# Kernel optimization log

Hardware: AMD Instinct MI355X
Metric: run time of the kernel (lower is better)

## Reference

```python
import jax, jax.numpy as jnp
import numpy as np

B, T, D, H = 4096, 256, 5, 64


def setup_inputs() -> dict:
    key = jax.random.key(0)
    ks = jax.random.split(key, 11)
    s = 1.0 / np.sqrt(H)  # PyTorch default init scale
    mk = lambda k, shape: jax.random.uniform(k, shape, jnp.float32, -s, s)
    return {
        "x": jax.random.normal(ks[0], (B, T, D), jnp.float32),
        "w_ih0": mk(ks[1], (3 * H, D)),
        "w_hh0": mk(ks[2], (3 * H, H)),
        "b_ih0": mk(ks[3], (3 * H,)),
        "b_hh0": mk(ks[4], (3 * H,)),
        "w_ih1": mk(ks[5], (3 * H, H)),
        "w_hh1": mk(ks[6], (3 * H, H)),
        "b_ih1": mk(ks[7], (3 * H,)),
        "b_hh1": mk(ks[8], (3 * H,)),
        "fc_w": mk(ks[9], (1, H)),
        "fc_b": mk(ks[10], (1,)),
    }


def _gru_layer(x, w_ih, w_hh, b_ih, b_hh):
    # x: [B, T, Din] -> outputs [B, T, H]. PyTorch gate order: r, z, n.
    h_dim = w_hh.shape[1]
    xg = jnp.einsum("btd,gd->btg", x, w_ih) + b_ih  # [B, T, 3H] (one big GEMM)

    def step(h, xg_t):
        hg = h @ w_hh.T + b_hh  # [B, 3H]
        xr, xz, xn = jnp.split(xg_t, 3, axis=-1)
        hr, hz, hn = jnp.split(hg, 3, axis=-1)
        r = jax.nn.sigmoid(xr + hr)
        z = jax.nn.sigmoid(xz + hz)
        n = jnp.tanh(xn + r * hn)
        h_new = (1.0 - z) * n + z * h
        return h_new, h_new

    h0 = jnp.zeros((x.shape[0], h_dim), x.dtype)
    _, hs = jax.lax.scan(step, h0, jnp.swapaxes(xg, 0, 1))  # hs: [T, B, H]
    return jnp.swapaxes(hs, 0, 1)


def reference(x, w_ih0, w_hh0, b_ih0, b_hh0, w_ih1, w_hh1, b_ih1, b_hh1, fc_w, fc_b):
    h1 = _gru_layer(x, w_ih0, w_hh0, b_ih0, b_hh0)   # [B, T, H]
    h2 = _gru_layer(h1, w_ih1, w_hh1, b_ih1, b_hh1)  # [B, T, H]
    last = h2[:, -1, :]                               # [B, H]
    return last @ fc_w.T + fc_b                       # [B, 1]
```

## Files before the change

### kernel.cpp

```cpp
#include <hip/hip_runtime.h>
#include <hip/hip_bf16.h>


typedef __attribute__((ext_vector_type(8))) _Float16 f16x8;
typedef __attribute__((ext_vector_type(4))) float f32x4;

#define MFMA16(a, b, c) __builtin_amdgcn_mfma_f32_16x16x32_f16(a, b, c, 0, 0, 0)

#define T_SZ 256
#define HB   72
#define NLOG2E  (-1.4426950408889634f)
#define PLOG2E  ( 1.4426950408889634f)
#define N2LOG2E (-2.8853900817779268f)

__device__ __forceinline__ void load_wfrag_hi(const float* __restrict__ W, int grow,
                                              int kbase, float scale, f16x8& hi) {
#pragma unroll
    for (int j = 0; j < 8; ++j)
        hi[j] = (_Float16)(W[grow * 64 + kbase + j] * scale);
}

__global__ __launch_bounds__(1024, 1)
void gru2_16w(const float* __restrict__ x,
              const float* __restrict__ w_ih0, const float* __restrict__ w_hh0,
              const float* __restrict__ b_ih0, const float* __restrict__ b_hh0,
              const float* __restrict__ w_ih1, const float* __restrict__ w_hh1,
              const float* __restrict__ b_ih1, const float* __restrict__ b_hh1,
              const float* __restrict__ fc_w, const float* __restrict__ fc_b,
              float* __restrict__ out)
{
    __shared__ __align__(16) _Float16 xhi[T_SZ][16][8];
    __shared__ __align__(16) _Float16 h0hi[2][16][HB];
    __shared__ __align__(16) _Float16 h1hi[2][16][HB];
    __shared__ __align__(16) float    pP[2][3][64][20];
    __shared__ __align__(16) float    xnB[2][64][20];

    const int tid  = threadIdx.x;
    const int lane = tid & 63;
    const int wave = tid >> 6;
    const int grp  = wave >> 2;
    const int wl   = wave & 3;
    const int u    = lane & 15;
    const int kq   = lane >> 4;
    const int ug   = wl * 16 + u;
    const int rbase = 4 * kq;

    {
        const float* xsrc = x + (size_t)blockIdx.x * (16 * 1280);
        for (int idx = tid; idx < 16 * 1280; idx += 1024) {
            int row = idx / 1280;
            int rem = idx - row * 1280;
            int t   = rem / 5;
            int d   = rem - t * 5;
            xhi[t][row][d] = (_Float16)xsrc[idx];
        }
        for (int idx = tid; idx < T_SZ * 16; idx += 1024) {
            int t = idx >> 4, row = idx & 15;
            xhi[t][row][5] = (_Float16)0.0f;
            xhi[t][row][6] = (_Float16)0.0f;
            xhi[t][row][7] = (_Float16)0.0f;
        }
        for (int idx = tid; idx < 2 * 16 * HB; idx += 1024) {
            ((_Float16*)h0hi)[idx] = (_Float16)0.0f;
            ((_Float16*)h1hi)[idx] = (_Float16)0.0f;
        }
    }
    __syncthreads();

    if (grp == 0) {
        f16x8 wR[2], wZ[2], wN[2];
#pragma unroll
        for (int kk = 0; kk < 2; ++kk) {
            const int kb = kk * 32 + 8 * kq;
            load_wfrag_hi(w_hh0, 0 * 64 + ug, kb, NLOG2E,  wR[kk]);
            load_wfrag_hi(w_hh0, 1 * 64 + ug, kb, PLOG2E,  wZ[kk]);
            load_wfrag_hi(w_hh0, 2 * 64 + ug, kb, N2LOG2E, wN[kk]);
        }
        f16x8 bxR, bxZ;
#pragma unroll
        for (int j = 0; j < 8; ++j) { bxR[j] = (_Float16)0.0f; bxZ[j] = (_Float16)0.0f; }
        if (kq == 0) {
#pragma unroll
            for (int j = 0; j < 5; ++j) {
                bxR[j] = (_Float16)(w_ih0[(0 * 64 + ug) * 5 + j] * NLOG2E);
                bxZ[j] = (_Float16)(w_ih0[(1 * 64 + ug) * 5 + j] * PLOG2E);
            }
        }
        const float bR0  = (b_ih0[ug] + b_hh0[ug]) * NLOG2E;
        const float bZ0  = (b_ih0[64 + ug] + b_hh0[64 + ug]) * PLOG2E;
        const float bXN0 = b_ih0[128 + ug] * N2LOG2E;
        const float bHN0 = b_hh0[128 + ug] * N2LOG2E;
        float h0_own[4] = {0.f, 0.f, 0.f, 0.f};

        float xn_pro[4];
        {
            float wxn[5];
#pragma unroll
            for (int d = 0; d < 5; ++d) wxn[d] = w_ih0[(128 + ug) * 5 + d] * N2LOG2E;
#pragma unroll
            for (int r = 0; r < 4; ++r) {
                const float* xp = x + ((size_t)(blockIdx.x * 16 + rbase + r) * T_SZ) * 5;
                float vN = bXN0;
#pragma unroll
                for (int d = 0; d < 5; ++d) vN = fmaf(wxn[d], xp[d], vN);
                xn_pro[r] = vN;
            }
        }

        for (int i = 0; i <= T_SZ + 1; ++i) {
            if (i < T_SZ) {
                const int pr = (i + 1) & 1, ps = i & 1;
                f16x8 xf;
#pragma unroll
                for (int j = 0; j < 8; ++j) xf[j] = (_Float16)0.0f;
                if (kq == 0) xf = *(const f16x8*)&xhi[i][u][0];
                f16x8 ah[2];
                ah[0] = *(const f16x8*)&h0hi[pr][u][8 * kq];
                ah[1] = *(const f16x8*)&h0hi[pr][u][32 + 8 * kq];
                f32x4 aR  = {bR0, bR0, bR0, bR0};
                f32x4 aZ  = {bZ0, bZ0, bZ0, bZ0};
                f32x4 aNa = {bHN0, bHN0, bHN0, bHN0};
                f32x4 aNb = {0.f, 0.f, 0.f, 0.f};
                __builtin_amdgcn_s_setprio(1);
                aR  = MFMA16(xf, bxR, aR);
                aZ  = MFMA16(xf, bxZ, aZ);
                aNa = MFMA16(ah[0], wN[0], aNa);
                aNb = MFMA16(ah[1], wN[1], aNb);
                aR  = MFMA16(ah[0], wR[0], aR);
                aZ  = MFMA16(ah[0], wZ[0], aZ);
                aR  = MFMA16(ah[1], wR[1], aR);
                aZ  = MFMA16(ah[1], wZ[1], aZ);
                __builtin_amdgcn_s_setprio(0);
                float xn0[4];
                if (i == 0) {
#pragma unroll
                    for (int r = 0; r < 4; ++r) xn0[r] = xn_pro[r];
                } else {
                    const f32x4 q = *(const f32x4*)&xnB[i & 1][ug][rbase];
#pragma unroll
                    for (int r = 0; r < 4; ++r) xn0[r] = q[r];
                }
#pragma unroll
                for (int r = 0; r < 4; ++r) {
                    float ER = __builtin_amdgcn_exp2f(aR[r]);
                    float rg = __builtin_amdgcn_rcpf(1.0f + ER);
                    float w  = fmaf(rg, aNa[r] + aNb[r], xn0[r]);
                    float EN = __builtin_amdgcn_exp2f(w);
                    float n  = fmaf(2.0f, __builtin_amdgcn_rcpf(1.0f + EN), -1.0f);
                    float EZ = __builtin_amdgcn_exp2f(aZ[r]);
                    float hv = fmaf(EZ, h0_own[r], n) * __builtin_amdgcn_rcpf(1.0f + EZ);
                    h0_own[r] = hv;
                    h0hi[ps][rbase + r][ug] = (_Float16)hv;
                }
            }
            __syncthreads();
        }
    } else if (grp == 1) {
        f16x8 iR[2], iZ[2], iX[2];
#pragma unroll
        for (int kk = 0; kk < 2; ++kk) {
            const int kb = kk * 32 + 8 * kq;
            load_wfrag_hi(w_ih1, 0 * 64 + ug, kb, NLOG2E,  iR[kk]);
            load_wfrag_hi(w_ih1, 1 * 64 + ug, kb, PLOG2E,  iZ[kk]);
            load_wfrag_hi(w_ih1, 2 * 64 + ug, kb, N2LOG2E, iX[kk]);
        }
        const float bR1 = (b_ih1[ug] + b_hh1[ug]) * NLOG2E;
        const float bZ1 = (b_ih1[64 + ug] + b_hh1[64 + ug]) * PLOG2E;
        const float bX1 = b_ih1[128 + ug] * N2LOG2E;

        for (int i = 0; i <= T_SZ + 1; ++i) {
            if (i >= 1 && i <= T_SZ) {
                const int t = i - 1, st = t & 1;
                f16x8 ah[2];
                ah[0] = *(const f16x8*)&h0hi[st][u][8 * kq];
                ah[1] = *(const f16x8*)&h0hi[st][u][32 + 8 * kq];
                f32x4 qR = {bR1, bR1, bR1, bR1};
                f32x4 qZ = {bZ1, bZ1, bZ1, bZ1};
                f32x4 qXa = {bX1, bX1, bX1, bX1};
                f32x4 qXb = {0.f, 0.f, 0.f, 0.f};
                qR  = MFMA16(ah[0], iR[0], qR);
                qZ  = MFMA16(ah[0], iZ[0], qZ);
                qXa = MFMA16(ah[0], iX[0], qXa);
                qXb = MFMA16(ah[1], iX[1], qXb);
                qR  = MFMA16(ah[1], iR[1], qR);
                qZ  = MFMA16(ah[1], iZ[1], qZ);
#pragma unroll
                for (int r = 0; r < 4; ++r) qXa[r] += qXb[r];
                *(f32x4*)&pP[st][0][ug][rbase] = qR;
                *(f32x4*)&pP[st][1][ug][rbase] = qZ;
                *(f32x4*)&pP[st][2][ug][rbase] = qXa;
            }
            __syncthreads();
        }
    } else if (grp == 2) {
        float wxn[5];
#pragma unroll
        for (int d = 0; d < 5; ++d) wxn[d] = w_ih0[(128 + ug) * 5 + d] * N2LOG2E;
        const float bXN0 = b_ih0[128 + ug] * N2LOG2E;

        for (int i = 0; i <= T_SZ + 1; ++i) {
            if (i <= T_SZ - 2) {
                f32x4 xnv;
#pragma unroll
                for (int r = 0; r < 4; ++r) {
                    const float* xp = x + ((size_t)(blockIdx.x * 16 + rbase + r) * T_SZ + (i + 1)) * 5;
                    float vN = bXN0;
#pragma unroll
                    for (int d = 0; d < 5; ++d) vN = fmaf(wxn[d], xp[d], vN);
                    xnv[r] = vN;
                }
                *(f32x4*)&xnB[(i + 1) & 1][ug][rbase] = xnv;
            }
            __syncthreads();
        }
    } else {
        f16x8 hR[2], hZ[2], hN[2];
#pragma unroll
        for (int kk = 0; kk < 2; ++kk) {
            const int kb = kk * 32 + 8 * kq;
            load_wfrag_hi(w_hh1, 0 * 64 + ug, kb, NLOG2E,  hR[kk]);
            load_wfrag_hi(w_hh1, 1 * 64 + ug, kb, PLOG2E,  hZ[kk]);
            load_wfrag_hi(w_hh1, 2 * 64 + ug, kb, N2LOG2E, hN[kk]);
        }
        const float bN1 = b_hh1[128 + ug] * N2LOG2E;
        float h1_own[4] = {0.f, 0.f, 0.f, 0.f};

        for (int i = 0; i <= T_SZ + 1; ++i) {
            if (i >= 2) {
                const int t = i - 2, st = t & 1;
                f16x8 ah[2];
                ah[0] = *(const f16x8*)&h1hi[st ^ 1][u][8 * kq];
                ah[1] = *(const f16x8*)&h1hi[st ^ 1][u][32 + 8 * kq];
                const f32x4 qR = *(const f32x4*)&pP[st][0][ug][rbase];
                const f32x4 qZ = *(const f32x4*)&pP[st][1][ug][rbase];
                const f32x4 qX = *(const f32x4*)&pP[st][2][ug][rbase];
                f32x4 cR = {0.f, 0.f, 0.f, 0.f};
                f32x4 cZ = {0.f, 0.f, 0.f, 0.f};
                f32x4 cNa = {bN1, bN1, bN1, bN1};
                f32x4 cNb = {0.f, 0.f, 0.f, 0.f};
                __builtin_amdgcn_s_setprio(1);
                cR  = MFMA16(ah[0], hR[0], cR);
                cZ  = MFMA16(ah[0], hZ[0], cZ);
                cNa = MFMA16(ah[0], hN[0], cNa);
                cNb = MFMA16(ah[1], hN[1], cNb);
                cR  = MFMA16(ah[1], hR[1], cR);
                cZ  = MFMA16(ah[1], hZ[1], cZ);
                __builtin_amdgcn_s_setprio(0);
#pragma unroll
                for (int r = 0; r < 4; ++r) {
                    float ER = __builtin_amdgcn_exp2f(cR[r] + qR[r]);
                    float rg = __builtin_amdgcn_rcpf(1.0f + ER);
                    float w  = fmaf(rg, cNa[r] + cNb[r], qX[r]);
                    float EN = __builtin_amdgcn_exp2f(w);
                    float n  = fmaf(2.0f, __builtin_amdgcn_rcpf(1.0f + EN), -1.0f);
                    float EZ = __builtin_amdgcn_exp2f(cZ[r] + qZ[r]);
                    float hv = fmaf(EZ, h1_own[r], n) * __builtin_amdgcn_rcpf(1.0f + EZ);
                    h1_own[r] = hv;
                    h1hi[st][rbase + r][ug] = (_Float16)hv;
                }
            }
            __syncthreads();
        }
    }

    if (tid < 16) {
        float s = fc_b[0];
#pragma unroll 1
        for (int uu = 0; uu < 64; ++uu)
            s = fmaf(fc_w[uu], (float)h1hi[1][tid][uu], s);
        out[blockIdx.x * 16 + tid] = s;
    }
}

extern "C" void kernel_launch(void* const* d_in, const int* in_sizes, int n_in,
                              void* d_out, int out_size, void* d_ws, size_t ws_size,
                              hipStream_t stream) {
    const float* x     = (const float*)d_in[0];
    const float* w_ih0 = (const float*)d_in[1];
    const float* w_hh0 = (const float*)d_in[2];
    const float* b_ih0 = (const float*)d_in[3];
    const float* b_hh0 = (const float*)d_in[4];
    const float* w_ih1 = (const float*)d_in[5];
    const float* w_hh1 = (const float*)d_in[6];
    const float* b_ih1 = (const float*)d_in[7];
    const float* b_hh1 = (const float*)d_in[8];
    const float* fc_w  = (const float*)d_in[9];
    const float* fc_b  = (const float*)d_in[10];
    float* out = (float*)d_out;

    gru2_16w<<<dim3(256), dim3(1024), 0, stream>>>(x, w_ih0, w_hh0, b_ih0, b_hh0,
                                                   w_ih1, w_hh1, b_ih1, b_hh1,
                                                   fc_w, fc_b, out);
}
```

Before: 161.2 us.

## Move layer-0 input projections for all gates to the helper wave group

Layer-0 input projections for the r and z gates are now computed in fp32 by the helper group (grp 2), alongside the n gate it already handled. They are double-buffered through shared memory and loaded as the accumulator initial values, which removes two MFMAs from the serial recurrence step of layer 0. The shared-memory staging of x as fp16 and its prologue transpose are dropped, cutting startup cost. In exchange the helper group does three times the FMAs, global loads and shared-memory stores per step, and the recurrent wave reads two extra f32x4 values from LDS each step.

```diff
diff --git a/kernel.cpp b/kernel.cpp
--- a/kernel.cpp
+++ b/kernel.cpp
@@ -21,19 +21,18 @@
 }
 
 __global__ __launch_bounds__(1024, 1)
-void gru2_16w(const float* __restrict__ x,
-              const float* __restrict__ w_ih0, const float* __restrict__ w_hh0,
-              const float* __restrict__ b_ih0, const float* __restrict__ b_hh0,
-              const float* __restrict__ w_ih1, const float* __restrict__ w_hh1,
-              const float* __restrict__ b_ih1, const float* __restrict__ b_hh1,
-              const float* __restrict__ fc_w, const float* __restrict__ fc_b,
-              float* __restrict__ out)
+void gru2_slim0(const float* __restrict__ x,
+                const float* __restrict__ w_ih0, const float* __restrict__ w_hh0,
+                const float* __restrict__ b_ih0, const float* __restrict__ b_hh0,
+                const float* __restrict__ w_ih1, const float* __restrict__ w_hh1,
+                const float* __restrict__ b_ih1, const float* __restrict__ b_hh1,
+                const float* __restrict__ fc_w, const float* __restrict__ fc_b,
+                float* __restrict__ out)
 {
-    __shared__ __align__(16) _Float16 xhi[T_SZ][16][8];
     __shared__ __align__(16) _Float16 h0hi[2][16][HB];
     __shared__ __align__(16) _Float16 h1hi[2][16][HB];
     __shared__ __align__(16) float    pP[2][3][64][20];
-    __shared__ __align__(16) float    xnB[2][64][20];
+    __shared__ __align__(16) float    xA[2][3][64][20];
 
     const int tid  = threadIdx.x;
     const int lane = tid & 63;
@@ -45,25 +44,9 @@
     const int ug   = wl * 16 + u;
     const int rbase = 4 * kq;
 
-    {
-        const float* xsrc = x + (size_t)blockIdx.x * (16 * 1280);
-        for (int idx = tid; idx < 16 * 1280; idx += 1024) {
-            int row = idx / 1280;
-            int rem = idx - row * 1280;
-            int t   = rem / 5;
-            int d   = rem - t * 5;
-            xhi[t][row][d] = (_Float16)xsrc[idx];
-        }
-        for (int idx = tid; idx < T_SZ * 16; idx += 1024) {
-            int t = idx >> 4, row = idx & 15;
-            xhi[t][row][5] = (_Float16)0.0f;
-            xhi[t][row][6] = (_Float16)0.0f;
-            xhi[t][row][7] = (_Float16)0.0f;
-        }
-        for (int idx = tid; idx < 2 * 16 * HB; idx += 1024) {
-            ((_Float16*)h0hi)[idx] = (_Float16)0.0f;
-            ((_Float16*)h1hi)[idx] = (_Float16)0.0f;
-        }
+    for (int idx = tid; idx < 2 * 16 * HB; idx += 1024) {
+        ((_Float16*)h0hi)[idx] = (_Float16)0.0f;
+        ((_Float16*)h1hi)[idx] = (_Float16)0.0f;
     }
     __syncthreads();
 
@@ -76,54 +59,58 @@
             load_wfrag_hi(w_hh0, 1 * 64 + ug, kb, PLOG2E,  wZ[kk]);
             load_wfrag_hi(w_hh0, 2 * 64 + ug, kb, N2LOG2E, wN[kk]);
         }
-        f16x8 bxR, bxZ;
-#pragma unroll
-        for (int j = 0; j < 8; ++j) { bxR[j] = (_Float16)0.0f; bxZ[j] = (_Float16)0.0f; }
-        if (kq == 0) {
-#pragma unroll
-            for (int j = 0; j < 5; ++j) {
-                bxR[j] = (_Float16)(w_ih0[(0 * 64 + ug) * 5 + j] * NLOG2E);
-                bxZ[j] = (_Float16)(w_ih0[(1 * 64 + ug) * 5 + j] * PLOG2E);
-            }
-        }
-        const float bR0  = (b_ih0[ug] + b_hh0[ug]) * NLOG2E;
-        const float bZ0  = (b_ih0[64 + ug] + b_hh0[64 + ug]) * PLOG2E;
-        const float bXN0 = b_ih0[128 + ug] * N2LOG2E;
         const float bHN0 = b_hh0[128 + ug] * N2LOG2E;
         float h0_own[4] = {0.f, 0.f, 0.f, 0.f};
 
-        float xn_pro[4];
+        f32x4 proR, proZ, proX;
         {
-            float wxn[5];
-#pragma unroll
-            for (int d = 0; d < 5; ++d) wxn[d] = w_ih0[(128 + ug) * 5 + d] * N2LOG2E;
+            float wxr[5], wxz[5], wxn[5];
+#pragma unroll
+            for (int d = 0; d < 5; ++d) {
+                wxr[d] = w_ih0[(0 * 64 + ug) * 5 + d] * NLOG2E;
+                wxz[d] = w_ih0[(1 * 64 + ug) * 5 + d] * PLOG2E;
+                wxn[d] = w_ih0[(128 + ug) * 5 + d] * N2LOG2E;
+            }
+            const float bR0  = (b_ih0[ug] + b_hh0[ug]) * NLOG2E;
+            const float bZ0  = (b_ih0[64 + ug] + b_hh0[64 + ug]) * PLOG2E;
+            const float bXN0 = b_ih0[128 + ug] * N2LOG2E;
 #pragma unroll
             for (int r = 0; r < 4; ++r) {
                 const float* xp = x + ((size_t)(blockIdx.x * 16 + rbase + r) * T_SZ) * 5;
-                float vN = bXN0;
-#pragma unroll
-                for (int d = 0; d < 5; ++d) vN = fmaf(wxn[d], xp[d], vN);
-                xn_pro[r] = vN;
+                float vR = bR0, vZ = bZ0, vN = bXN0;
+#pragma unroll
+                for (int d = 0; d < 5; ++d) {
+                    float x1 = xp[d];
+                    vR = fmaf(wxr[d], x1, vR);
+                    vZ = fmaf(wxz[d], x1, vZ);
+                    vN = fmaf(wxn[d], x1, vN);
+                }
+                proR[r] = vR; proZ[r] = vZ; proX[r] = vN;
             }
         }
 
         for (int i = 0; i <= T_SZ + 1; ++i) {
             if (i < T_SZ) {
                 const int pr = (i + 1) & 1, ps = i & 1;
-                f16x8 xf;
-#pragma unroll
-                for (int j = 0; j < 8; ++j) xf[j] = (_Float16)0.0f;
-                if (kq == 0) xf = *(const f16x8*)&xhi[i][u][0];
                 f16x8 ah[2];
                 ah[0] = *(const f16x8*)&h0hi[pr][u][8 * kq];
                 ah[1] = *(const f16x8*)&h0hi[pr][u][32 + 8 * kq];
-                f32x4 aR  = {bR0, bR0, bR0, bR0};
-                f32x4 aZ  = {bZ0, bZ0, bZ0, bZ0};
-                f32x4 aNa = {bHN0, bHN0, bHN0, bHN0};
-                f32x4 aNb = {0.f, 0.f, 0.f, 0.f};
+                f32x4 aR, aZ, aNa, aNb;
+                float xn0[4];
+                if (i == 0) {
+                    aR = proR; aZ = proZ;
+#pragma unroll
+                    for (int r = 0; r < 4; ++r) xn0[r] = proX[r];
+                } else {
+                    aR = *(const f32x4*)&xA[i & 1][0][ug][rbase];
+                    aZ = *(const f32x4*)&xA[i & 1][1][ug][rbase];
+                    const f32x4 q = *(const f32x4*)&xA[i & 1][2][ug][rbase];
+#pragma unroll
+                    for (int r = 0; r < 4; ++r) xn0[r] = q[r];
+                }
+#pragma unroll
+                for (int r = 0; r < 4; ++r) { aNa[r] = bHN0; aNb[r] = 0.f; }
                 __builtin_amdgcn_s_setprio(1);
-                aR  = MFMA16(xf, bxR, aR);
-                aZ  = MFMA16(xf, bxZ, aZ);
                 aNa = MFMA16(ah[0], wN[0], aNa);
                 aNb = MFMA16(ah[1], wN[1], aNb);
                 aR  = MFMA16(ah[0], wR[0], aR);
@@ -131,15 +118,6 @@
                 aR  = MFMA16(ah[1], wR[1], aR);
                 aZ  = MFMA16(ah[1], wZ[1], aZ);
                 __builtin_amdgcn_s_setprio(0);
-                float xn0[4];
-                if (i == 0) {
-#pragma unroll
-                    for (int r = 0; r < 4; ++r) xn0[r] = xn_pro[r];
-                } else {
-                    const f32x4 q = *(const f32x4*)&xnB[i & 1][ug][rbase];
-#pragma unroll
-                    for (int r = 0; r < 4; ++r) xn0[r] = q[r];
-                }
 #pragma unroll
                 for (int r = 0; r < 4; ++r) {
                     float ER = __builtin_amdgcn_exp2f(aR[r]);
@@ -193,23 +171,37 @@
             __syncthreads();
         }
     } else if (grp == 2) {
-        float wxn[5];
-#pragma unroll
-        for (int d = 0; d < 5; ++d) wxn[d] = w_ih0[(128 + ug) * 5 + d] * N2LOG2E;
+        float wxr[5], wxz[5], wxn[5];
+#pragma unroll
+        for (int d = 0; d < 5; ++d) {
+            wxr[d] = w_ih0[(0 * 64 + ug) * 5 + d] * NLOG2E;
+            wxz[d] = w_ih0[(1 * 64 + ug) * 5 + d] * PLOG2E;
+            wxn[d] = w_ih0[(128 + ug) * 5 + d] * N2LOG2E;
+        }
+        const float bR0  = (b_ih0[ug] + b_hh0[ug]) * NLOG2E;
+        const float bZ0  = (b_ih0[64 + ug] + b_hh0[64 + ug]) * PLOG2E;
         const float bXN0 = b_ih0[128 + ug] * N2LOG2E;
 
         for (int i = 0; i <= T_SZ + 1; ++i) {
             if (i <= T_SZ - 2) {
-                f32x4 xnv;
+                f32x4 xvR, xvZ, xvN;
 #pragma unroll
                 for (int r = 0; r < 4; ++r) {
                     const float* xp = x + ((size_t)(blockIdx.x * 16 + rbase + r) * T_SZ + (i + 1)) * 5;
-                    float vN = bXN0;
-#pragma unroll
-                    for (int d = 0; d < 5; ++d) vN = fmaf(wxn[d], xp[d], vN);
-                    xnv[r] = vN;
-                }
-                *(f32x4*)&xnB[(i + 1) & 1][ug][rbase] = xnv;
+                    float vR = bR0, vZ = bZ0, vN = bXN0;
+#pragma unroll
+                    for (int d = 0; d < 5; ++d) {
+                        float x1 = xp[d];
+                        vR = fmaf(wxr[d], x1, vR);
+                        vZ = fmaf(wxz[d], x1, vZ);
+                        vN = fmaf(wxn[d], x1, vN);
+                    }
+                    xvR[r] = vR; xvZ[r] = vZ; xvN[r] = vN;
+                }
+                const int sl = (i + 1) & 1;
+                *(f32x4*)&xA[sl][0][ug][rbase] = xvR;
+                *(f32x4*)&xA[sl][1][ug][rbase] = xvZ;
+                *(f32x4*)&xA[sl][2][ug][rbase] = xvN;
             }
             __syncthreads();
         }
@@ -288,7 +280,7 @@
     const float* fc_b  = (const float*)d_in[10];
     float* out = (float*)d_out;
 
-    gru2_16w<<<dim3(256), dim3(1024), 0, stream>>>(x, w_ih0, w_hh0, b_ih0, b_hh0,
-                                                   w_ih1, w_hh1, b_ih1, b_hh1,
-                                                   fc_w, fc_b, out);
+    gru2_slim0<<<dim3(256), dim3(1024), 0, stream>>>(x, w_ih0, w_hh0, b_ih0, b_hh0,
+                                                     w_ih1, w_hh1, b_ih1, b_hh1,
+                                                     fc_w, fc_b, out);
 }
```

Result: slower. 167.8 us (+4.1%).
